# Performance work log

Measured on AMD Instinct MI355X. Metric: run time of the kernel, lower is better.

The kernel has to match this reference:

```python
import jax, jax.numpy as jnp
import numpy as np

B, T, E = 4096, 200, 64
H1, H2 = 80, 40  # att_hidden_units


def setup_inputs() -> dict:
    key = jax.random.key(0)
    ks = jax.random.split(key, 9)
    glorot = jax.nn.initializers.glorot_normal()
    return {
        "queries": jax.random.normal(ks[0], (B, 1, E), jnp.float32),
        "keys": jax.random.normal(ks[1], (B, T, E), jnp.float32),
        "keys_length": jax.random.randint(ks[2], (B, 1), 0, T, jnp.int32),
        "W1": glorot(ks[3], (2 * E, H1), jnp.float32),
        "b1": jnp.zeros((H1,), jnp.float32),
        "W2": glorot(ks[4], (H1, H2), jnp.float32),
        "b2": jnp.zeros((H2,), jnp.float32),
        "kernel": glorot(ks[5], (H2, 1), jnp.float32),
        "bias": jnp.zeros((1,), jnp.float32),
    }


def reference(queries, keys, keys_length, W1, b1, W2, b2, kernel, bias):
    b, t, e = keys.shape
    # tile query across all T key positions and concat -> (B, T, 2E)
    q = jnp.broadcast_to(queries, (b, t, e))
    att_input = jnp.concatenate([q, keys], axis=-1)
    # local activation unit: small per-key MLP with sigmoid activations
    h = jax.nn.sigmoid(att_input @ W1 + b1)   # (B, T, H1)
    h = jax.nn.sigmoid(h @ W2 + b2)           # (B, T, H2)
    score = h @ kernel + bias                 # (B, T, 1)
    scores = jnp.transpose(score, (0, 2, 1))  # (B, 1, T)
    # sequence mask from keys_length (B, 1)
    mask = jnp.arange(t)[None, None, :] < keys_length[:, :, None]  # (B, 1, T)
    paddings = jnp.full_like(scores, -(2.0 ** 32) + 1.0)
    scores = jnp.where(mask, scores, paddings)
    # weight_normalization=True -> softmax over T
    weights = jax.nn.softmax(scores, axis=-1)  # (B, 1, T)
    # weighted-sum pooling over keys -> (B, 1, E)
    out = jnp.matmul(weights, keys)
    return out
```

## Files before the change

kernel.cpp:

```cpp
#include <hip/hip_runtime.h>
#include <hip/hip_bf16.h>

#define TT 200
#define EE 64
#define NT 7

typedef unsigned short u16;
typedef unsigned int u32;
typedef __attribute__((ext_vector_type(8))) short bfrag;
typedef __attribute__((ext_vector_type(4))) float f32x4;

__device__ __forceinline__ u16 f2bf(float f) {
    __hip_bfloat16 h(f);
    return __builtin_bit_cast(u16, h);
}
__device__ __forceinline__ float bf2f(u16 h) {
    return __uint_as_float(((u32)h) << 16);
}
__device__ __forceinline__ float sigmoid_fast(float x) {
    return __builtin_amdgcn_rcpf(1.0f + __expf(-x));
}

__global__ void prep_frags(const float* __restrict__ W1, const float* __restrict__ W2,
                           u16* __restrict__ A1p, u16* __restrict__ A2p,
                           u16* __restrict__ A1q) {
    int idx = blockIdx.x * 256 + threadIdx.x;
    if (idx < 5 * 2 * 64 * 8) {
        int j = idx & 7, l = (idx >> 3) & 63, ks = (idx >> 9) & 1, mt5 = idx >> 10;
        int g = l >> 4, m = mt5 * 16 + (l & 15);
        int k = ks * 32 + g * 8 + j;
        A1p[idx] = f2bf(W1[(64 + k) * 80 + m]);
        A1q[idx] = f2bf(W1[k * 80 + m]);
    }
    if (idx < 3 * 3 * 64 * 8) {
        int j = idx & 7, l = (idx >> 3) & 63, ks = (idx >> 9) % 3, m2 = idx / 1536;
        int g = l >> 4, m = m2 * 16 + (l & 15);
        int i24 = ks * 8 + j;
        u16 v = 0;
        if (i24 < 20 && m < 40) {
            int mt5 = i24 >> 2, r = i24 & 3;
            int k = mt5 * 16 + g * 4 + r;
            v = f2bf(W2[k * 40 + m]);
        }
        A2p[idx] = v;
    }
}

#define LOADK32(MT, QA0, QA1, QA2, QA3, QB0, QB1, QB2, QB3) {           \
    int ra_ = (MT) * 32 + l15;                                          \
    QA0 = QA1 = QA2 = QA3 = make_float4(0.f, 0.f, 0.f, 0.f);            \
    QB0 = QB1 = QB2 = QB3 = make_float4(0.f, 0.f, 0.f, 0.f);            \
    if (ra_ < lenEff) {                                                 \
        const float* p_ = kb + ra_ * EE + g * 8;                        \
        QA0 = *reinterpret_cast<const float4*>(p_);                     \
        QA1 = *reinterpret_cast<const float4*>(p_ + 4);                 \
        QA2 = *reinterpret_cast<const float4*>(p_ + 32);                \
        QA3 = *reinterpret_cast<const float4*>(p_ + 36);                \
    }                                                                   \
    if (ra_ + 16 < lenEff) {                                            \
        const float* p_ = kb + (ra_ + 16) * EE + g * 8;                 \
        QB0 = *reinterpret_cast<const float4*>(p_);                     \
        QB1 = *reinterpret_cast<const float4*>(p_ + 4);                 \
        QB2 = *reinterpret_cast<const float4*>(p_ + 32);                \
        QB3 = *reinterpret_cast<const float4*>(p_ + 36);                \
    } }

#define PACK(A, X, Y) {                                                 \
    A[0] = (short)f2bf(X.x); A[1] = (short)f2bf(X.y);                   \
    A[2] = (short)f2bf(X.z); A[3] = (short)f2bf(X.w);                   \
    A[4] = (short)f2bf(Y.x); A[5] = (short)f2bf(Y.y);                   \
    A[6] = (short)f2bf(Y.z); A[7] = (short)f2bf(Y.w); }

__global__ __launch_bounds__(256, 2) void din_mfma(
    const float* __restrict__ queries,
    const float* __restrict__ keys,
    const int*   __restrict__ keys_length,
    const float* __restrict__ b1,
    const float* __restrict__ b2,
    const float* __restrict__ wk,
    const float* __restrict__ bias,
    const u16*   __restrict__ A1p,
    const u16*   __restrict__ A2p,
    const u16*   __restrict__ A1q,
    float* __restrict__ out)
{
    __shared__ __align__(16) u16 w1ls[5 * 2 * 64 * 8];
    __shared__ __align__(16) u16 w2ls[3 * 3 * 64 * 8];
    __shared__ __align__(16) float wkls[48];
    __shared__ __align__(16) float b2ls[48];
    __shared__ __align__(16) float qils[4][80];

    const int tid  = threadIdx.x;
    const int lane = tid & 63;
    const int wv   = tid >> 6;
    const int l15  = lane & 15;
    const int g    = lane >> 4;
    const int b    = blockIdx.x * 4 + wv;

    const float* kb = keys + (size_t)b * (TT * EE);
    const float* q  = queries + (size_t)b * EE;
    const int len   = keys_length[b];
    const float biass = bias[0];

    const int lenEff = (len == 0) ? TT : len;
    const int ntiles = (lenEff + 31) >> 5;

    for (int c = tid; c < 640; c += 256)
        *reinterpret_cast<float4*>(&w1ls[c * 8]) = reinterpret_cast<const float4*>(A1p)[c];
    for (int c = tid; c < 576; c += 256)
        *reinterpret_cast<float4*>(&w2ls[c * 8]) = reinterpret_cast<const float4*>(A2p)[c];
    if (tid < 48) {
        wkls[tid] = (tid < 40) ? wk[tid] : 0.f;
        b2ls[tid] = (tid < 40) ? b2[tid] : 0.f;
    }

    {
        bfrag qf0, qf1;
        const float* qp = q + g * 8;
        float4 q0 = *reinterpret_cast<const float4*>(qp);
        float4 q1 = *reinterpret_cast<const float4*>(qp + 4);
        float4 q2 = *reinterpret_cast<const float4*>(qp + 32);
        float4 q3 = *reinterpret_cast<const float4*>(qp + 36);
        PACK(qf0, q0, q1); PACK(qf1, q2, q3);
        #pragma unroll
        for (int mt5 = 0; mt5 < 5; ++mt5) {
            bfrag aq0 = *reinterpret_cast<const bfrag*>(A1q + (((mt5 * 2 + 0) * 64 + lane) << 3));
            bfrag aq1 = *reinterpret_cast<const bfrag*>(A1q + (((mt5 * 2 + 1) * 64 + lane) << 3));
            f32x4 c = { 0.f, 0.f, 0.f, 0.f };
            c = __builtin_amdgcn_mfma_f32_16x16x32_bf16(aq0, qf0, c, 0, 0, 0);
            c = __builtin_amdgcn_mfma_f32_16x16x32_bf16(aq1, qf1, c, 0, 0, 0);
            float4 bv = *reinterpret_cast<const float4*>(b1 + mt5 * 16 + g * 4);
            if (l15 == 0) {
                float4 o = { c[0] + bv.x, c[1] + bv.y, c[2] + bv.z, c[3] + bv.w };
                *reinterpret_cast<float4*>(&qils[wv][mt5 * 16 + g * 4]) = o;
            }
        }
    }
    __syncthreads();

    float acc[16];
    #pragma unroll
    for (int j = 0; j < 16; ++j) acc[j] = 0.f;
    float Z = 0.f;

    float4 qa0, qa1, qa2, qa3, qb0, qb1_, qb2, qb3;
    LOADK32(0, qa0, qa1, qa2, qa3, qb0, qb1_, qb2, qb3);
    bfrag a0, a1, a2, a3;
    PACK(a0, qa0, qa1); PACK(a1, qa2, qa3);
    PACK(a2, qb0, qb1_); PACK(a3, qb2, qb3);

    for (int mt = 0; mt < ntiles; ++mt) {
        if (mt + 1 < ntiles) { LOADK32(mt + 1, qa0, qa1, qa2, qa3, qb0, qb1_, qb2, qb3); }

        bfrag xa0, xa1, xa2, xb0, xb1, xb2;
        {
            f32x4 d[5];
            #pragma unroll
            for (int mt5 = 0; mt5 < 5; ++mt5) {
                bfrag wA = *reinterpret_cast<const bfrag*>(&w1ls[((mt5 * 2 + 0) * 64 + lane) * 8]);
                bfrag wB = *reinterpret_cast<const bfrag*>(&w1ls[((mt5 * 2 + 1) * 64 + lane) * 8]);
                f32x4 c = *reinterpret_cast<const f32x4*>(&qils[wv][mt5 * 16 + g * 4]);
                c = __builtin_amdgcn_mfma_f32_16x16x32_bf16(wA, a0, c, 0, 0, 0);
                c = __builtin_amdgcn_mfma_f32_16x16x32_bf16(wB, a1, c, 0, 0, 0);
                d[mt5] = c;
            }
            #pragma unroll
            for (int j = 0; j < 8; ++j) {
                xa0[j] = (short)f2bf(sigmoid_fast(d[j >> 2][j & 3]));
                xa1[j] = (short)f2bf(sigmoid_fast(d[(8 + j) >> 2][(8 + j) & 3]));
                xa2[j] = (short)((16 + j) < 20
                            ? f2bf(sigmoid_fast(d[(16 + j) >> 2][(16 + j) & 3])) : 0);
            }
        }
        {
            f32x4 d[5];
            #pragma unroll
            for (int mt5 = 0; mt5 < 5; ++mt5) {
                bfrag wA = *reinterpret_cast<const bfrag*>(&w1ls[((mt5 * 2 + 0) * 64 + lane) * 8]);
                bfrag wB = *reinterpret_cast<const bfrag*>(&w1ls[((mt5 * 2 + 1) * 64 + lane) * 8]);
                f32x4 c = *reinterpret_cast<const f32x4*>(&qils[wv][mt5 * 16 + g * 4]);
                c = __builtin_amdgcn_mfma_f32_16x16x32_bf16(wA, a2, c, 0, 0, 0);
                c = __builtin_amdgcn_mfma_f32_16x16x32_bf16(wB, a3, c, 0, 0, 0);
                d[mt5] = c;
            }
            #pragma unroll
            for (int j = 0; j < 8; ++j) {
                xb0[j] = (short)f2bf(sigmoid_fast(d[j >> 2][j & 3]));
                xb1[j] = (short)f2bf(sigmoid_fast(d[(8 + j) >> 2][(8 + j) & 3]));
                xb2[j] = (short)((16 + j) < 20
                            ? f2bf(sigmoid_fast(d[(16 + j) >> 2][(16 + j) & 3])) : 0);
            }
        }

        float pa = 0.f, pb = 0.f;
        #pragma unroll
        for (int m2 = 0; m2 < 3; ++m2) {
            bfrag u0 = *reinterpret_cast<const bfrag*>(&w2ls[((m2 * 3 + 0) * 64 + lane) * 8]);
            bfrag u1 = *reinterpret_cast<const bfrag*>(&w2ls[((m2 * 3 + 1) * 64 + lane) * 8]);
            bfrag u2 = *reinterpret_cast<const bfrag*>(&w2ls[((m2 * 3 + 2) * 64 + lane) * 8]);
            f32x4 ci = *reinterpret_cast<const f32x4*>(&b2ls[m2 * 16 + g * 4]);
            f32x4 wv4 = *reinterpret_cast<const f32x4*>(&wkls[m2 * 16 + g * 4]);
            f32x4 ca = ci, cb = ci;
            ca = __builtin_amdgcn_mfma_f32_16x16x32_bf16(u0, xa0, ca, 0, 0, 0);
            ca = __builtin_amdgcn_mfma_f32_16x16x32_bf16(u1, xa1, ca, 0, 0, 0);
            ca = __builtin_amdgcn_mfma_f32_16x16x32_bf16(u2, xa2, ca, 0, 0, 0);
            cb = __builtin_amdgcn_mfma_f32_16x16x32_bf16(u0, xb0, cb, 0, 0, 0);
            cb = __builtin_amdgcn_mfma_f32_16x16x32_bf16(u1, xb1, cb, 0, 0, 0);
            cb = __builtin_amdgcn_mfma_f32_16x16x32_bf16(u2, xb2, cb, 0, 0, 0);
            #pragma unroll
            for (int rr = 0; rr < 4; ++rr) {
                pa = fmaf(sigmoid_fast(ca[rr]), wv4[rr], pa);
                pb = fmaf(sigmoid_fast(cb[rr]), wv4[rr], pb);
            }
        }
        pa += __shfl_xor(pa, 16); pa += __shfl_xor(pa, 32);
        pb += __shfl_xor(pb, 16); pb += __shfl_xor(pb, 32);

        const int ra = mt * 32 + l15, rb = ra + 16;
        float ea = (ra < len) ? __expf(pa + biass) : ((len == 0 && ra < TT) ? 1.f : 0.f);
        float eb = (rb < len) ? __expf(pb + biass) : ((len == 0 && rb < TT) ? 1.f : 0.f);
        Z += ea + eb;

        #pragma unroll
        for (int j = 0; j < 8; ++j) {
            acc[j]     = fmaf(ea, bf2f((u16)a0[j]), fmaf(eb, bf2f((u16)a2[j]), acc[j]));
            acc[8 + j] = fmaf(ea, bf2f((u16)a1[j]), fmaf(eb, bf2f((u16)a3[j]), acc[8 + j]));
        }

        if (mt + 1 < ntiles) {
            PACK(a0, qa0, qa1); PACK(a1, qa2, qa3);
            PACK(a2, qb0, qb1_); PACK(a3, qb2, qb3);
        }
    }

    Z += __shfl_xor(Z, 1); Z += __shfl_xor(Z, 2);
    Z += __shfl_xor(Z, 4); Z += __shfl_xor(Z, 8);
    #pragma unroll
    for (int j = 0; j < 16; ++j) {
        acc[j] += __shfl_xor(acc[j], 1);
        acc[j] += __shfl_xor(acc[j], 2);
        acc[j] += __shfl_xor(acc[j], 4);
        acc[j] += __shfl_xor(acc[j], 8);
    }
    if (l15 == 0) {
        float inv = __builtin_amdgcn_rcpf(Z);
        float* ob = out + (size_t)b * EE + g * 8;
        float4 o0 = { acc[0] * inv,  acc[1] * inv,  acc[2] * inv,  acc[3] * inv };
        float4 o1 = { acc[4] * inv,  acc[5] * inv,  acc[6] * inv,  acc[7] * inv };
        float4 o2 = { acc[8] * inv,  acc[9] * inv,  acc[10] * inv, acc[11] * inv };
        float4 o3 = { acc[12] * inv, acc[13] * inv, acc[14] * inv, acc[15] * inv };
        *reinterpret_cast<float4*>(ob)      = o0;
        *reinterpret_cast<float4*>(ob + 4)  = o1;
        *reinterpret_cast<float4*>(ob + 32) = o2;
        *reinterpret_cast<float4*>(ob + 36) = o3;
    }
}

extern "C" void kernel_launch(void* const* d_in, const int* in_sizes, int n_in,
                              void* d_out, int out_size, void* d_ws, size_t ws_size,
                              hipStream_t stream) {
    const float* queries = (const float*)d_in[0];
    const float* keys    = (const float*)d_in[1];
    const int*   klen    = (const int*)d_in[2];
    const float* W1      = (const float*)d_in[3];
    const float* b1      = (const float*)d_in[4];
    const float* W2      = (const float*)d_in[5];
    const float* b2      = (const float*)d_in[6];
    const float* wk      = (const float*)d_in[7];
    const float* bias    = (const float*)d_in[8];
    float* out           = (float*)d_out;

    u16* A1p = (u16*)d_ws;
    u16* A2p = (u16*)((char*)d_ws + 10240);
    u16* A1q = (u16*)((char*)d_ws + 19456);

    prep_frags<<<20, 256, 0, stream>>>(W1, W2, A1p, A2p, A1q);
    din_mfma<<<1024, 256, 0, stream>>>(queries, keys, klen, b1, b2, wk, bias,
                                       A1p, A2p, A1q, out);
}
```

Before: 50.91 us.

## Split each batch row's key tiles across four waves with LDS reduction

Changes the mapping so each block processes one batch row, with its four waves taking interleaved 32-key tiles, instead of one row per wave. Partial softmax numerators and denominators are combined through shared memory before the final normalization and store. This is meant to reduce per-wave serial latency and load imbalance from varying key lengths. In exchange it launches four times as many blocks, each repeating the weight staging into LDS, and adds a block barrier and reduction.

```diff
diff --git a/kernel.cpp b/kernel.cpp
--- a/kernel.cpp
+++ b/kernel.cpp
@@ -3,7 +3,6 @@
 
 #define TT 200
 #define EE 64
-#define NT 7
 
 typedef unsigned short u16;
 typedef unsigned int u32;
@@ -89,13 +88,15 @@
     __shared__ __align__(16) float wkls[48];
     __shared__ __align__(16) float b2ls[48];
     __shared__ __align__(16) float qils[4][80];
+    __shared__ __align__(16) float redls[4][64];
+    __shared__ float zls[4];
 
     const int tid  = threadIdx.x;
     const int lane = tid & 63;
     const int wv   = tid >> 6;
     const int l15  = lane & 15;
     const int g    = lane >> 4;
-    const int b    = blockIdx.x * 4 + wv;
+    const int b    = blockIdx.x;
 
     const float* kb = keys + (size_t)b * (TT * EE);
     const float* q  = queries + (size_t)b * EE;
@@ -144,13 +145,13 @@
     float Z = 0.f;
 
     float4 qa0, qa1, qa2, qa3, qb0, qb1_, qb2, qb3;
-    LOADK32(0, qa0, qa1, qa2, qa3, qb0, qb1_, qb2, qb3);
+    LOADK32(wv, qa0, qa1, qa2, qa3, qb0, qb1_, qb2, qb3);
     bfrag a0, a1, a2, a3;
     PACK(a0, qa0, qa1); PACK(a1, qa2, qa3);
     PACK(a2, qb0, qb1_); PACK(a3, qb2, qb3);
 
-    for (int mt = 0; mt < ntiles; ++mt) {
-        if (mt + 1 < ntiles) { LOADK32(mt + 1, qa0, qa1, qa2, qa3, qb0, qb1_, qb2, qb3); }
+    for (int mt = wv; mt < ntiles; mt += 4) {
+        if (mt + 4 < ntiles) { LOADK32(mt + 4, qa0, qa1, qa2, qa3, qb0, qb1_, qb2, qb3); }
 
         bfrag xa0, xa1, xa2, xb0, xb1, xb2;
         {
@@ -227,7 +228,7 @@
             acc[8 + j] = fmaf(ea, bf2f((u16)a1[j]), fmaf(eb, bf2f((u16)a3[j]), acc[8 + j]));
         }
 
-        if (mt + 1 < ntiles) {
+        if (mt + 4 < ntiles) {
             PACK(a0, qa0, qa1); PACK(a1, qa2, qa3);
             PACK(a2, qb0, qb1_); PACK(a3, qb2, qb3);
         }
@@ -243,16 +244,18 @@
         acc[j] += __shfl_xor(acc[j], 8);
     }
     if (l15 == 0) {
-        float inv = __builtin_amdgcn_rcpf(Z);
-        float* ob = out + (size_t)b * EE + g * 8;
-        float4 o0 = { acc[0] * inv,  acc[1] * inv,  acc[2] * inv,  acc[3] * inv };
-        float4 o1 = { acc[4] * inv,  acc[5] * inv,  acc[6] * inv,  acc[7] * inv };
-        float4 o2 = { acc[8] * inv,  acc[9] * inv,  acc[10] * inv, acc[11] * inv };
-        float4 o3 = { acc[12] * inv, acc[13] * inv, acc[14] * inv, acc[15] * inv };
-        *reinterpret_cast<float4*>(ob)      = o0;
-        *reinterpret_cast<float4*>(ob + 4)  = o1;
-        *reinterpret_cast<float4*>(ob + 32) = o2;
-        *reinterpret_cast<float4*>(ob + 36) = o3;
+        #pragma unroll
+        for (int j = 0; j < 16; ++j) redls[wv][g * 16 + j] = acc[j];
+        if (lane == 0) zls[wv] = Z;
+    }
+    __syncthreads();
+    if (tid < 64) {
+        int gg = (tid & 31) >> 3;
+        int jj = (tid & 7) + ((tid >> 5) << 3);
+        int idx = gg * 16 + jj;
+        float s = (redls[0][idx] + redls[1][idx]) + (redls[2][idx] + redls[3][idx]);
+        float Zt = (zls[0] + zls[1]) + (zls[2] + zls[3]);
+        out[(size_t)b * EE + tid] = s * __builtin_amdgcn_rcpf(Zt);
     }
 }
 
@@ -275,6 +278,6 @@
     u16* A1q = (u16*)((char*)d_ws + 19456);
 
     prep_frags<<<20, 256, 0, stream>>>(W1, W2, A1p, A2p, A1q);
-    din_mfma<<<1024, 256, 0, stream>>>(queries, keys, klen, b1, b2, wk, bias,
+    din_mfma<<<4096, 256, 0, stream>>>(queries, keys, klen, b1, b2, wk, bias,
                                        A1p, A2p, A1q, out);
 }
```

Result: slower. 73.61 us (+44.6%).

## Precompute query-bias projection in separate kernel and skip empty half-tiles

Applied to the files above, without the earlier changes.

Moves the per-batch query·W1 + b1 MFMA projection out of the main kernel into a new prep_qb1 kernel that writes an 80-float table per batch row. The main kernel loads it into shared memory. The main loop also adds a branch that skips the second 16-row half of a 32-row tile when it lies entirely past the valid length, avoiding its layer-1 MFMAs, sigmoids and layer-2 MFMAs. The cost is an extra kernel launch and a global round trip for the table, plus code duplication and a wave-uniform branch.

```diff
diff --git a/kernel.cpp b/kernel.cpp
--- a/kernel.cpp
+++ b/kernel.cpp
@@ -3,7 +3,6 @@
 
 #define TT 200
 #define EE 64
-#define NT 7
 
 typedef unsigned short u16;
 typedef unsigned int u32;
@@ -43,6 +42,43 @@
             v = f2bf(W2[k * 40 + m]);
         }
         A2p[idx] = v;
+    }
+}
+
+#define PACK(A, X, Y) {                                                 \
+    A[0] = (short)f2bf(X.x); A[1] = (short)f2bf(X.y);                   \
+    A[2] = (short)f2bf(X.z); A[3] = (short)f2bf(X.w);                   \
+    A[4] = (short)f2bf(Y.x); A[5] = (short)f2bf(Y.y);                   \
+    A[6] = (short)f2bf(Y.z); A[7] = (short)f2bf(Y.w); }
+
+__global__ __launch_bounds__(256) void prep_qb1(
+    const float* __restrict__ queries, const float* __restrict__ b1,
+    const u16* __restrict__ A1q, float* __restrict__ qb1tab) {
+    const int lane = threadIdx.x & 63;
+    const int wv   = threadIdx.x >> 6;
+    const int l15  = lane & 15;
+    const int g    = lane >> 4;
+    const int b    = blockIdx.x * 4 + wv;
+
+    const float* qp = queries + (size_t)b * EE + g * 8;
+    float4 q0 = *reinterpret_cast<const float4*>(qp);
+    float4 q1 = *reinterpret_cast<const float4*>(qp + 4);
+    float4 q2 = *reinterpret_cast<const float4*>(qp + 32);
+    float4 q3 = *reinterpret_cast<const float4*>(qp + 36);
+    bfrag qf0, qf1;
+    PACK(qf0, q0, q1); PACK(qf1, q2, q3);
+    #pragma unroll
+    for (int mt5 = 0; mt5 < 5; ++mt5) {
+        bfrag aq0 = *reinterpret_cast<const bfrag*>(A1q + (((mt5 * 2 + 0) * 64 + lane) << 3));
+        bfrag aq1 = *reinterpret_cast<const bfrag*>(A1q + (((mt5 * 2 + 1) * 64 + lane) << 3));
+        f32x4 c = { 0.f, 0.f, 0.f, 0.f };
+        c = __builtin_amdgcn_mfma_f32_16x16x32_bf16(aq0, qf0, c, 0, 0, 0);
+        c = __builtin_amdgcn_mfma_f32_16x16x32_bf16(aq1, qf1, c, 0, 0, 0);
+        float4 bv = *reinterpret_cast<const float4*>(b1 + mt5 * 16 + g * 4);
+        if (l15 == 0) {
+            float4 o = { c[0] + bv.x, c[1] + bv.y, c[2] + bv.z, c[3] + bv.w };
+            *reinterpret_cast<float4*>(qb1tab + (size_t)b * 80 + mt5 * 16 + g * 4) = o;
+        }
     }
 }
 
@@ -65,23 +101,15 @@
         QB3 = *reinterpret_cast<const float4*>(p_ + 36);                \
     } }
 
-#define PACK(A, X, Y) {                                                 \
-    A[0] = (short)f2bf(X.x); A[1] = (short)f2bf(X.y);                   \
-    A[2] = (short)f2bf(X.z); A[3] = (short)f2bf(X.w);                   \
-    A[4] = (short)f2bf(Y.x); A[5] = (short)f2bf(Y.y);                   \
-    A[6] = (short)f2bf(Y.z); A[7] = (short)f2bf(Y.w); }
-
 __global__ __launch_bounds__(256, 2) void din_mfma(
-    const float* __restrict__ queries,
     const float* __restrict__ keys,
     const int*   __restrict__ keys_length,
-    const float* __restrict__ b1,
     const float* __restrict__ b2,
     const float* __restrict__ wk,
     const float* __restrict__ bias,
     const u16*   __restrict__ A1p,
     const u16*   __restrict__ A2p,
-    const u16*   __restrict__ A1q,
+    const float* __restrict__ qb1tab,
     float* __restrict__ out)
 {
     __shared__ __align__(16) u16 w1ls[5 * 2 * 64 * 8];
@@ -98,7 +126,6 @@
     const int b    = blockIdx.x * 4 + wv;
 
     const float* kb = keys + (size_t)b * (TT * EE);
-    const float* q  = queries + (size_t)b * EE;
     const int len   = keys_length[b];
     const float biass = bias[0];
 
@@ -113,29 +140,9 @@
         wkls[tid] = (tid < 40) ? wk[tid] : 0.f;
         b2ls[tid] = (tid < 40) ? b2[tid] : 0.f;
     }
-
-    {
-        bfrag qf0, qf1;
-        const float* qp = q + g * 8;
-        float4 q0 = *reinterpret_cast<const float4*>(qp);
-        float4 q1 = *reinterpret_cast<const float4*>(qp + 4);
-        float4 q2 = *reinterpret_cast<const float4*>(qp + 32);
-        float4 q3 = *reinterpret_cast<const float4*>(qp + 36);
-        PACK(qf0, q0, q1); PACK(qf1, q2, q3);
-        #pragma unroll
-        for (int mt5 = 0; mt5 < 5; ++mt5) {
-            bfrag aq0 = *reinterpret_cast<const bfrag*>(A1q + (((mt5 * 2 + 0) * 64 + lane) << 3));
-            bfrag aq1 = *reinterpret_cast<const bfrag*>(A1q + (((mt5 * 2 + 1) * 64 + lane) << 3));
-            f32x4 c = { 0.f, 0.f, 0.f, 0.f };
-            c = __builtin_amdgcn_mfma_f32_16x16x32_bf16(aq0, qf0, c, 0, 0, 0);
-            c = __builtin_amdgcn_mfma_f32_16x16x32_bf16(aq1, qf1, c, 0, 0, 0);
-            float4 bv = *reinterpret_cast<const float4*>(b1 + mt5 * 16 + g * 4);
-            if (l15 == 0) {
-                float4 o = { c[0] + bv.x, c[1] + bv.y, c[2] + bv.z, c[3] + bv.w };
-                *reinterpret_cast<float4*>(&qils[wv][mt5 * 16 + g * 4]) = o;
-            }
-        }
-    }
+    if (lane < 20)
+        *reinterpret_cast<float4*>(&qils[wv][lane * 4]) =
+            *reinterpret_cast<const float4*>(qb1tab + (size_t)b * 80 + lane * 4);
     __syncthreads();
 
     float acc[16];
@@ -151,8 +158,9 @@
 
     for (int mt = 0; mt < ntiles; ++mt) {
         if (mt + 1 < ntiles) { LOADK32(mt + 1, qa0, qa1, qa2, qa3, qb0, qb1_, qb2, qb3); }
-
-        bfrag xa0, xa1, xa2, xb0, xb1, xb2;
+        const bool hasB = (mt * 32 + 16) < lenEff;
+
+        bfrag xa0, xa1, xa2;
         {
             f32x4 d[5];
             #pragma unroll
@@ -172,59 +180,85 @@
                             ? f2bf(sigmoid_fast(d[(16 + j) >> 2][(16 + j) & 3])) : 0);
             }
         }
-        {
-            f32x4 d[5];
-            #pragma unroll
-            for (int mt5 = 0; mt5 < 5; ++mt5) {
-                bfrag wA = *reinterpret_cast<const bfrag*>(&w1ls[((mt5 * 2 + 0) * 64 + lane) * 8]);
-                bfrag wB = *reinterpret_cast<const bfrag*>(&w1ls[((mt5 * 2 + 1) * 64 + lane) * 8]);
-                f32x4 c = *reinterpret_cast<const f32x4*>(&qils[wv][mt5 * 16 + g * 4]);
-                c = __builtin_amdgcn_mfma_f32_16x16x32_bf16(wA, a2, c, 0, 0, 0);
-                c = __builtin_amdgcn_mfma_f32_16x16x32_bf16(wB, a3, c, 0, 0, 0);
-                d[mt5] = c;
-            }
+
+        float pa = 0.f, pb = 0.f, ea, eb = 0.f;
+        const int ra = mt * 32 + l15, rb = ra + 16;
+
+        if (hasB) {
+            bfrag xb0, xb1, xb2;
+            {
+                f32x4 d[5];
+                #pragma unroll
+                for (int mt5 = 0; mt5 < 5; ++mt5) {
+                    bfrag wA = *reinterpret_cast<const bfrag*>(&w1ls[((mt5 * 2 + 0) * 64 + lane) * 8]);
+                    bfrag wB = *reinterpret_cast<const bfrag*>(&w1ls[((mt5 * 2 + 1) * 64 + lane) * 8]);
+                    f32x4 c = *reinterpret_cast<const f32x4*>(&qils[wv][mt5 * 16 + g * 4]);
+                    c = __builtin_amdgcn_mfma_f32_16x16x32_bf16(wA, a2, c, 0, 0, 0);
+                    c = __builtin_amdgcn_mfma_f32_16x16x32_bf16(wB, a3, c, 0, 0, 0);
+                    d[mt5] = c;
+                }
+                #pragma unroll
+                for (int j = 0; j < 8; ++j) {
+                    xb0[j] = (short)f2bf(sigmoid_fast(d[j >> 2][j & 3]));
+                    xb1[j] = (short)f2bf(sigmoid_fast(d[(8 + j) >> 2][(8 + j) & 3]));
+                    xb2[j] = (short)((16 + j) < 20
+                                ? f2bf(sigmoid_fast(d[(16 + j) >> 2][(16 + j) & 3])) : 0);
+                }
+            }
+            #pragma unroll
+            for (int m2 = 0; m2 < 3; ++m2) {
+                bfrag u0 = *reinterpret_cast<const bfrag*>(&w2ls[((m2 * 3 + 0) * 64 + lane) * 8]);
+                bfrag u1 = *reinterpret_cast<const bfrag*>(&w2ls[((m2 * 3 + 1) * 64 + lane) * 8]);
+                bfrag u2 = *reinterpret_cast<const bfrag*>(&w2ls[((m2 * 3 + 2) * 64 + lane) * 8]);
+                f32x4 ci = *reinterpret_cast<const f32x4*>(&b2ls[m2 * 16 + g * 4]);
+                f32x4 wv4 = *reinterpret_cast<const f32x4*>(&wkls[m2 * 16 + g * 4]);
+                f32x4 ca = ci, cb = ci;
+                ca = __builtin_amdgcn_mfma_f32_16x16x32_bf16(u0, xa0, ca, 0, 0, 0);
+                ca = __builtin_amdgcn_mfma_f32_16x16x32_bf16(u1, xa1, ca, 0, 0, 0);
+                ca = __builtin_amdgcn_mfma_f32_16x16x32_bf16(u2, xa2, ca, 0, 0, 0);
+                cb = __builtin_amdgcn_mfma_f32_16x16x32_bf16(u0, xb0, cb, 0, 0, 0);
+                cb = __builtin_amdgcn_mfma_f32_16x16x32_bf16(u1, xb1, cb, 0, 0, 0);
+                cb = __builtin_amdgcn_mfma_f32_16x16x32_bf16(u2, xb2, cb, 0, 0, 0);
+                #pragma unroll
+                for (int rr = 0; rr < 4; ++rr) {
+                    pa = fmaf(sigmoid_fast(ca[rr]), wv4[rr], pa);
+                    pb = fmaf(sigmoid_fast(cb[rr]), wv4[rr], pb);
+                }
+            }
+            pa += __shfl_xor(pa, 16); pa += __shfl_xor(pa, 32);
+            pb += __shfl_xor(pb, 16); pb += __shfl_xor(pb, 32);
+            ea = (ra < len) ? __expf(pa + biass) : ((len == 0 && ra < TT) ? 1.f : 0.f);
+            eb = (rb < len) ? __expf(pb + biass) : ((len == 0 && rb < TT) ? 1.f : 0.f);
+            Z += ea + eb;
             #pragma unroll
             for (int j = 0; j < 8; ++j) {
-                xb0[j] = (short)f2bf(sigmoid_fast(d[j >> 2][j & 3]));
-                xb1[j] = (short)f2bf(sigmoid_fast(d[(8 + j) >> 2][(8 + j) & 3]));
-                xb2[j] = (short)((16 + j) < 20
-                            ? f2bf(sigmoid_fast(d[(16 + j) >> 2][(16 + j) & 3])) : 0);
-            }
-        }
-
-        float pa = 0.f, pb = 0.f;
-        #pragma unroll
-        for (int m2 = 0; m2 < 3; ++m2) {
-            bfrag u0 = *reinterpret_cast<const bfrag*>(&w2ls[((m2 * 3 + 0) * 64 + lane) * 8]);
-            bfrag u1 = *reinterpret_cast<const bfrag*>(&w2ls[((m2 * 3 + 1) * 64 + lane) * 8]);
-            bfrag u2 = *reinterpret_cast<const bfrag*>(&w2ls[((m2 * 3 + 2) * 64 + lane) * 8]);
-            f32x4 ci = *reinterpret_cast<const f32x4*>(&b2ls[m2 * 16 + g * 4]);
-            f32x4 wv4 = *reinterpret_cast<const f32x4*>(&wkls[m2 * 16 + g * 4]);
-            f32x4 ca = ci, cb = ci;
-            ca = __builtin_amdgcn_mfma_f32_16x16x32_bf16(u0, xa0, ca, 0, 0, 0);
-            ca = __builtin_amdgcn_mfma_f32_16x16x32_bf16(u1, xa1, ca, 0, 0, 0);
-            ca = __builtin_amdgcn_mfma_f32_16x16x32_bf16(u2, xa2, ca, 0, 0, 0);
-            cb = __builtin_amdgcn_mfma_f32_16x16x32_bf16(u0, xb0, cb, 0, 0, 0);
-            cb = __builtin_amdgcn_mfma_f32_16x16x32_bf16(u1, xb1, cb, 0, 0, 0);
-            cb = __builtin_amdgcn_mfma_f32_16x16x32_bf16(u2, xb2, cb, 0, 0, 0);
-            #pragma unroll
-            for (int rr = 0; rr < 4; ++rr) {
-                pa = fmaf(sigmoid_fast(ca[rr]), wv4[rr], pa);
-                pb = fmaf(sigmoid_fast(cb[rr]), wv4[rr], pb);
-            }
-        }
-        pa += __shfl_xor(pa, 16); pa += __shfl_xor(pa, 32);
-        pb += __shfl_xor(pb, 16); pb += __shfl_xor(pb, 32);
-
-        const int ra = mt * 32 + l15, rb = ra + 16;
-        float ea = (ra < len) ? __expf(pa + biass) : ((len == 0 && ra < TT) ? 1.f : 0.f);
-        float eb = (rb < len) ? __expf(pb + biass) : ((len == 0 && rb < TT) ? 1.f : 0.f);
-        Z += ea + eb;
-
-        #pragma unroll
-        for (int j = 0; j < 8; ++j) {
-            acc[j]     = fmaf(ea, bf2f((u16)a0[j]), fmaf(eb, bf2f((u16)a2[j]), acc[j]));
-            acc[8 + j] = fmaf(ea, bf2f((u16)a1[j]), fmaf(eb, bf2f((u16)a3[j]), acc[8 + j]));
+                acc[j]     = fmaf(ea, bf2f((u16)a0[j]), fmaf(eb, bf2f((u16)a2[j]), acc[j]));
+                acc[8 + j] = fmaf(ea, bf2f((u16)a1[j]), fmaf(eb, bf2f((u16)a3[j]), acc[8 + j]));
+            }
+        } else {
+            #pragma unroll
+            for (int m2 = 0; m2 < 3; ++m2) {
+                bfrag u0 = *reinterpret_cast<const bfrag*>(&w2ls[((m2 * 3 + 0) * 64 + lane) * 8]);
+                bfrag u1 = *reinterpret_cast<const bfrag*>(&w2ls[((m2 * 3 + 1) * 64 + lane) * 8]);
+                bfrag u2 = *reinterpret_cast<const bfrag*>(&w2ls[((m2 * 3 + 2) * 64 + lane) * 8]);
+                f32x4 ci = *reinterpret_cast<const f32x4*>(&b2ls[m2 * 16 + g * 4]);
+                f32x4 wv4 = *reinterpret_cast<const f32x4*>(&wkls[m2 * 16 + g * 4]);
+                f32x4 ca = ci;
+                ca = __builtin_amdgcn_mfma_f32_16x16x32_bf16(u0, xa0, ca, 0, 0, 0);
+                ca = __builtin_amdgcn_mfma_f32_16x16x32_bf16(u1, xa1, ca, 0, 0, 0);
+                ca = __builtin_amdgcn_mfma_f32_16x16x32_bf16(u2, xa2, ca, 0, 0, 0);
+                #pragma unroll
+                for (int rr = 0; rr < 4; ++rr)
+                    pa = fmaf(sigmoid_fast(ca[rr]), wv4[rr], pa);
+            }
+            pa += __shfl_xor(pa, 16); pa += __shfl_xor(pa, 32);
+            ea = (ra < len) ? __expf(pa + biass) : ((len == 0 && ra < TT) ? 1.f : 0.f);
+            Z += ea;
+            #pragma unroll
+            for (int j = 0; j < 8; ++j) {
+                acc[j]     = fmaf(ea, bf2f((u16)a0[j]), acc[j]);
+                acc[8 + j] = fmaf(ea, bf2f((u16)a1[j]), acc[8 + j]);
+            }
         }
 
         if (mt + 1 < ntiles) {
@@ -270,11 +304,13 @@
     const float* bias    = (const float*)d_in[8];
     float* out           = (float*)d_out;
 
-    u16* A1p = (u16*)d_ws;
-    u16* A2p = (u16*)((char*)d_ws + 10240);
-    u16* A1q = (u16*)((char*)d_ws + 19456);
+    u16*   A1p    = (u16*)d_ws;
+    u16*   A2p    = (u16*)((char*)d_ws + 10240);
+    u16*   A1q    = (u16*)((char*)d_ws + 19456);
+    float* qb1tab = (float*)((char*)d_ws + 29696);
 
     prep_frags<<<20, 256, 0, stream>>>(W1, W2, A1p, A2p, A1q);
-    din_mfma<<<1024, 256, 0, stream>>>(queries, keys, klen, b1, b2, wk, bias,
-                                       A1p, A2p, A1q, out);
-}
+    prep_qb1<<<1024, 256, 0, stream>>>(queries, b1, A1q, qb1tab);
+    din_mfma<<<1024, 256, 0, stream>>>(keys, klen, b2, wk, bias,
+                                       A1p, A2p, qb1tab, out);
+}
```

After: 52.96 us. 1.04x slower.
